# Kernel tuning notes

Hardware: AMD Instinct MI355X
Metric: run time of the kernel (lower is better)

The kernel has to match this reference:

```python
import math
import jax, jax.numpy as jnp
import numpy as np

B, N, C = 2, 2048, 768
H, DH = 12, 64  # num_heads, head_dim


def setup_inputs() -> dict:
    key = jax.random.key(0)
    ks = jax.random.split(key, 5)
    s = 1.0 / math.sqrt(C)  # keep linear outputs O(1)
    return {
        "x": jax.random.normal(ks[0], (B, N, C), jnp.float32),
        "Wq": jax.random.normal(ks[1], (C, C), jnp.float32) * s,
        "bq": jnp.zeros((C,), jnp.float32),
        "Wk": jax.random.normal(ks[2], (C, C), jnp.float32) * s,
        "bk": jnp.zeros((C,), jnp.float32),
        "Wv": jax.random.normal(ks[3], (C, C), jnp.float32) * s,
        "bv": jnp.zeros((C,), jnp.float32),
        "Wp": jax.random.normal(ks[4], (C, C), jnp.float32) * s,
        "bp": jnp.zeros((C,), jnp.float32),
    }


def reference(x, Wq, bq, Wk, bk, Wv, bv, Wp, bp):
    # Linear projections; torch nn.Linear computes x @ W.T + b, here W stored
    # as (in, out) so it's x @ W + b with equivalent math.
    def split(t):  # [B,N,C] -> [B,H,N,DH]
        return t.reshape(B, N, H, DH).transpose(0, 2, 1, 3)

    q = split(x @ Wq + bq)
    k = split(x @ Wk + bk)
    v = split(x @ Wv + bv)
    scale = 1.0 / math.sqrt(DH)
    attn = jnp.einsum("bhqd,bhkd->bhqk", q, k) * scale  # [B,H,N,N]
    attn = jax.nn.softmax(attn, axis=-1)  # attn_drop=0.0 -> identity
    y = jnp.einsum("bhqk,bhkd->bhqd", attn, v)  # [B,H,N,DH]
    y = y.transpose(0, 2, 1, 3).reshape(B, N, C)
    return y @ Wp + bp  # proj_drop=0.0 -> identity
```

## Files before the change

### kernel.cpp

```cpp
#include <hip/hip_runtime.h>


typedef __bf16 bf16_t;
typedef __bf16 bf16x8 __attribute__((ext_vector_type(8)));
typedef __bf16 bf16x4 __attribute__((ext_vector_type(4)));
typedef short  short4_t __attribute__((ext_vector_type(4)));
typedef float  floatx4 __attribute__((ext_vector_type(4)));

#define MFMA32(a, b, c) __builtin_amdgcn_mfma_f32_16x16x32_bf16(a, b, c, 0, 0, 0)
#define MFMA16(a, b, c) __builtin_amdgcn_mfma_f32_16x16x16bf16_1k(a, b, c, 0, 0, 0)

__global__ __launch_bounds__(256) void cvt_x_kernel(const float* __restrict__ x,
                                                    bf16_t* __restrict__ xb) {
  int i = blockIdx.x * 256 + threadIdx.x;
  floatx4 v = ((const floatx4*)x)[i];
  bf16x4 o;
  o[0] = (bf16_t)v[0]; o[1] = (bf16_t)v[1]; o[2] = (bf16_t)v[2]; o[3] = (bf16_t)v[3];
  ((bf16x4*)xb)[i] = o;
}

__global__ __launch_bounds__(256) void cvt_wt_kernel(
    const float* __restrict__ W0, const float* __restrict__ W1,
    const float* __restrict__ W2, const float* __restrict__ W3,
    bf16_t* __restrict__ T0, bf16_t* __restrict__ T1,
    bf16_t* __restrict__ T2, bf16_t* __restrict__ T3) {
  const int z = blockIdx.z;
  const float* W = (z == 0) ? W0 : (z == 1) ? W1 : (z == 2) ? W2 : W3;
  bf16_t* WT = (z == 0) ? T0 : (z == 1) ? T1 : (z == 2) ? T2 : T3;
  __shared__ bf16_t T[64][65];
  const int c = threadIdx.x & 63, r0 = threadIdx.x >> 6;
  const int i0 = blockIdx.y * 64, o0 = blockIdx.x * 64;
#pragma unroll
  for (int p = 0; p < 16; ++p) {
    int r = p * 4 + r0;
    T[r][c] = (bf16_t)W[(i0 + r) * 768 + o0 + c];
  }
  __syncthreads();
#pragma unroll
  for (int p = 0; p < 16; ++p) {
    int r = p * 4 + r0;
    WT[(o0 + r) * 768 + i0 + c] = T[c][r];
  }
}

#define LDPG 72


__global__ __launch_bounds__(256) void gemm_qkv(
    const bf16_t* __restrict__ Xb, const bf16_t* __restrict__ WqT,
    const bf16_t* __restrict__ WkT, const bf16_t* __restrict__ WvT,
    const float* __restrict__ bq, const float* __restrict__ bk,
    const float* __restrict__ bv, bf16_t* __restrict__ qw,
    bf16_t* __restrict__ kw, bf16_t* __restrict__ vtw) {
  __shared__ bf16_t Al[128 * LDPG];
  __shared__ bf16_t Bl[128 * LDPG];
  const int z = blockIdx.z;
  const bf16_t* Wt = (z == 0) ? WqT : (z == 1) ? WkT : WvT;
  const float* bias = (z == 0) ? bq : (z == 1) ? bk : bv;
  const float oscale = (z == 0) ? 0.18033688011112042f : 1.0f;

  const int tid = threadIdx.x, lane = tid & 63, w = tid >> 6;
  const int wr = w >> 1, wc = w & 1;
  const int l15 = lane & 15, quad = lane >> 4;
  const int m0 = blockIdx.y * 128, n0 = blockIdx.x * 128;

  floatx4 acc[4][4] = {};

  for (int kt = 0; kt < 768; kt += 64) {
#pragma unroll
    for (int p = 0; p < 4; ++p) {
      int c = p * 256 + tid;
      int row = c >> 3, qo = (c & 7) * 8;
      *(bf16x8*)&Al[row * LDPG + qo] = *(const bf16x8*)&Wt[(m0 + row) * 768 + kt + qo];
      *(bf16x8*)&Bl[row * LDPG + qo] = *(const bf16x8*)&Xb[(n0 + row) * 768 + kt + qo];
    }
    __syncthreads();
#pragma unroll
    for (int kk = 0; kk < 2; ++kk) {
      bf16x8 af[4], bfr[4];
#pragma unroll
      for (int i = 0; i < 4; ++i) {
        af[i]  = *(bf16x8*)&Al[(wr * 64 + i * 16 + l15) * LDPG + kk * 32 + quad * 8];
        bfr[i] = *(bf16x8*)&Bl[(wc * 64 + i * 16 + l15) * LDPG + kk * 32 + quad * 8];
      }
#pragma unroll
      for (int mi = 0; mi < 4; ++mi)
#pragma unroll
        for (int ni = 0; ni < 4; ++ni)
          acc[mi][ni] = MFMA32(af[mi], bfr[ni], acc[mi][ni]);
    }
    __syncthreads();
  }

  const int hh = (m0 + wr * 64) >> 6;
#pragma unroll
  for (int mi = 0; mi < 4; ++mi) {
    const int d0 = mi * 16 + quad * 4;
    const int gm0 = m0 + wr * 64 + d0;
    float bv4[4];
#pragma unroll
    for (int r = 0; r < 4; ++r) bv4[r] = bias[gm0 + r];
#pragma unroll
    for (int ni = 0; ni < 4; ++ni) {
      const int gn = n0 + wc * 64 + ni * 16 + l15;
      const int bb = gn >> 11, tok = gn & 2047;
      const int bh = bb * 12 + hh;
      if (z == 0) {
        bf16x4 pk;
#pragma unroll
        for (int r = 0; r < 4; ++r)
          pk[r] = (bf16_t)((acc[mi][ni][r] + bv4[r]) * oscale);
        *(bf16x4*)&qw[bh * 131072 + tok * 64 + d0] = pk;
      } else if (z == 1) {
        const int kt2 = tok >> 7, k128 = tok & 127;
        const int nk = k128 >> 4, kl15 = k128 & 15;
        const int kk = d0 >> 5, kq = (d0 >> 3) & 3, j0 = d0 & 7;
        bf16x4 pk;
#pragma unroll
        for (int r = 0; r < 4; ++r)
          pk[r] = (bf16_t)(acc[mi][ni][r] + bv4[r]);
        *(bf16x4*)&kw[bh * 131072 + kt2 * 8192 +
                      ((nk * 2 + kk) * 64 + kq * 16 + kl15) * 8 + j0] = pk;
      } else {
        const int kt2 = tok >> 7, k128 = tok & 127;
        const int nk = k128 >> 4, vq = (k128 >> 2) & 3, j = k128 & 3;
        const int nd = d0 >> 4, vl0 = d0 & 15;
        const int base = bh * 131072 + kt2 * 8192 +
                         ((nk * 4 + nd) * 64 + vq * 16 + vl0) * 4 + j;
#pragma unroll
        for (int r = 0; r < 4; ++r)
          vtw[base + r * 4] = (bf16_t)(acc[mi][ni][r] + bv4[r]);
      }
    }
  }
}

__global__ __launch_bounds__(256) void gemm_proj(
    const bf16_t* __restrict__ Yb, const bf16_t* __restrict__ WpT,
    const float* __restrict__ bias, float* __restrict__ out) {
  __shared__ bf16_t Al[128 * LDPG];
  __shared__ bf16_t Bl[128 * LDPG];
  const int tid = threadIdx.x, lane = tid & 63, w = tid >> 6;
  const int wr = w >> 1, wc = w & 1;
  const int l15 = lane & 15, quad = lane >> 4;
  const int m0 = blockIdx.y * 128, n0 = blockIdx.x * 128;

  floatx4 acc[4][4] = {};

  for (int kt = 0; kt < 768; kt += 64) {
#pragma unroll
    for (int p = 0; p < 4; ++p) {
      int c = p * 256 + tid;
      int row = c >> 3, qo = (c & 7) * 8;
      *(bf16x8*)&Al[row * LDPG + qo] = *(const bf16x8*)&WpT[(m0 + row) * 768 + kt + qo];
      *(bf16x8*)&Bl[row * LDPG + qo] = *(const bf16x8*)&Yb[(n0 + row) * 768 + kt + qo];
    }
    __syncthreads();
#pragma unroll
    for (int kk = 0; kk < 2; ++kk) {
      bf16x8 af[4], bfr[4];
#pragma unroll
      for (int i = 0; i < 4; ++i) {
        af[i]  = *(bf16x8*)&Al[(wr * 64 + i * 16 + l15) * LDPG + kk * 32 + quad * 8];
        bfr[i] = *(bf16x8*)&Bl[(wc * 64 + i * 16 + l15) * LDPG + kk * 32 + quad * 8];
      }
#pragma unroll
      for (int mi = 0; mi < 4; ++mi)
#pragma unroll
        for (int ni = 0; ni < 4; ++ni)
          acc[mi][ni] = MFMA32(af[mi], bfr[ni], acc[mi][ni]);
    }
    __syncthreads();
  }

#pragma unroll
  for (int mi = 0; mi < 4; ++mi) {
    const int gm0 = m0 + wr * 64 + mi * 16 + quad * 4;
    floatx4 bv4;
#pragma unroll
    for (int r = 0; r < 4; ++r) bv4[r] = bias[gm0 + r];
#pragma unroll
    for (int ni = 0; ni < 4; ++ni) {
      const int gn = n0 + wc * 64 + ni * 16 + l15;
      floatx4 v = acc[mi][ni] + bv4;
      *(floatx4*)&out[gn * 768 + gm0] = v;
    }
  }
}

__global__ __launch_bounds__(256, 4) void attn_kernel(
    const bf16_t* __restrict__ Q, const bf16_t* __restrict__ Kf,
    const bf16_t* __restrict__ Vf, bf16_t* __restrict__ Y) {
  __shared__ __align__(16) bf16_t smem[16384];
  __shared__ float Ls[2][2][2][16];
  bf16_t* Kl = smem;
  bf16_t* Vl = smem + 8192;
  float* Ox = (float*)smem;

  const int tid = threadIdx.x, lane = tid & 63, w = tid >> 6;
  const int wq = w & 1, wk = w >> 1;
  const int l15 = lane & 15, quad = lane >> 4;
  const int bh = blockIdx.y;
  const int q0 = blockIdx.x * 64;
  const bf16_t* Qb = Q + bh * 131072;
  const bf16_t* Kb = Kf + bh * 131072;
  const bf16_t* Vb = Vf + bh * 131072;

  bf16x8 qf[2][2];
#pragma unroll
  for (int ni = 0; ni < 2; ++ni)
#pragma unroll
    for (int kk = 0; kk < 2; ++kk)
      qf[ni][kk] = *(const bf16x8*)&Qb[(q0 + wq * 32 + ni * 16 + l15) * 64 +
                                       kk * 32 + quad * 8];

  floatx4 oacc[2][4] = {};
  float lsum[2] = {0.f, 0.f};

  for (int kt = 0; kt < 16; ++kt) {
    const bf16_t* kg = Kb + kt * 8192;
    const bf16_t* vg = Vb + kt * 8192;
#pragma unroll
    for (int p = 0; p < 4; ++p) {
      const int off = (p * 256 + tid) * 8;
      *(bf16x8*)&Kl[off] = *(const bf16x8*)&kg[off];
      *(bf16x8*)&Vl[off] = *(const bf16x8*)&vg[off];
    }
    __syncthreads();

    short4_t pk[4][2];
#pragma unroll
    for (int mt = 0; mt < 4; ++mt) {
      floatx4 s[2] = {};
#pragma unroll
      for (int kk = 0; kk < 2; ++kk) {
        bf16x8 kfr = *(bf16x8*)&Kl[((wk * 4 + mt) * 2 + kk) * 512 + lane * 8];
#pragma unroll
        for (int ni = 0; ni < 2; ++ni)
          s[ni] = MFMA32(kfr, qf[ni][kk], s[ni]);
      }
#pragma unroll
      for (int ni = 0; ni < 2; ++ni) {
        bf16x4 ph;
#pragma unroll
        for (int r = 0; r < 4; ++r) {
          const float pv = __builtin_amdgcn_exp2f(s[ni][r]);
          lsum[ni] += pv;
          ph[r] = (bf16_t)pv;
        }
        pk[mt][ni] = __builtin_bit_cast(short4_t, ph);
      }
    }

#pragma unroll
    for (int mt = 0; mt < 4; ++mt)
#pragma unroll
      for (int nd = 0; nd < 4; ++nd) {
        bf16x4 vfr = *(bf16x4*)&Vl[((wk * 4 + mt) * 4 + nd) * 256 + lane * 4];
        short4_t vs = __builtin_bit_cast(short4_t, vfr);
#pragma unroll
        for (int ni = 0; ni < 2; ++ni)
          oacc[ni][nd] = MFMA16(pk[mt][ni], vs, oacc[ni][nd]);
      }
    __syncthreads();
  }

#pragma unroll
  for (int ni = 0; ni < 2; ++ni) {
    lsum[ni] += __shfl_xor(lsum[ni], 16);
    lsum[ni] += __shfl_xor(lsum[ni], 32);
  }
  if (quad == 0) {
#pragma unroll
    for (int ni = 0; ni < 2; ++ni) Ls[wq][wk][ni][l15] = lsum[ni];
  }

#pragma unroll
  for (int ni = 0; ni < 2; ++ni)
#pragma unroll
    for (int ndl = 0; ndl < 2; ++ndl) {
      const int nd = (1 - wk) * 2 + ndl;
      *(floatx4*)&Ox[((((wq * 2 + wk) * 2 + ni) * 2 + ndl) * 64 + lane) * 4] =
          oacc[ni][nd];
    }
  __syncthreads();

  const int bb = bh / 12, h = bh % 12;
#pragma unroll
  for (int ni = 0; ni < 2; ++ni) {
    float tot[4];
#pragma unroll
    for (int r = 0; r < 4; ++r)
      tot[r] = Ls[wq][0][ni][quad * 4 + r] + Ls[wq][1][ni][quad * 4 + r];
#pragma unroll
    for (int ndl = 0; ndl < 2; ++ndl) {
      const int nd = wk * 2 + ndl;
      floatx4 o = oacc[ni][nd];
      floatx4 other =
          *(floatx4*)&Ox[((((wq * 2 + (1 - wk)) * 2 + ni) * 2 + ndl) * 64 + lane) * 4];
      o += other;
#pragma unroll
      for (int r = 0; r < 4; ++r) {
        const int tok = q0 + wq * 32 + ni * 16 + quad * 4 + r;
        const int col = h * 64 + nd * 16 + l15;
        Y[(bb * 2048 + tok) * 768 + col] = (bf16_t)(o[r] / tot[r]);
      }
    }
  }
}

extern "C" void kernel_launch(void* const* d_in, const int* in_sizes, int n_in,
                              void* d_out, int out_size, void* d_ws, size_t ws_size,
                              hipStream_t stream) {
  const float* x  = (const float*)d_in[0];
  const float* Wq = (const float*)d_in[1];
  const float* bq = (const float*)d_in[2];
  const float* Wk = (const float*)d_in[3];
  const float* bk = (const float*)d_in[4];
  const float* Wv = (const float*)d_in[5];
  const float* bv = (const float*)d_in[6];
  const float* Wp = (const float*)d_in[7];
  const float* bp = (const float*)d_in[8];
  float* out = (float*)d_out;

  char* ws = (char*)d_ws;
  bf16_t* xb  = (bf16_t*)ws; ws += (size_t)4096 * 768 * 2;
  bf16_t* WqT = (bf16_t*)ws; ws += (size_t)768 * 768 * 2;
  bf16_t* WkT = (bf16_t*)ws; ws += (size_t)768 * 768 * 2;
  bf16_t* WvT = (bf16_t*)ws; ws += (size_t)768 * 768 * 2;
  bf16_t* WpT = (bf16_t*)ws; ws += (size_t)768 * 768 * 2;
  bf16_t* qw  = (bf16_t*)ws; ws += (size_t)24 * 2048 * 64 * 2;
  bf16_t* kw  = (bf16_t*)ws; ws += (size_t)24 * 2048 * 64 * 2;
  bf16_t* vtw = (bf16_t*)ws; ws += (size_t)24 * 2048 * 64 * 2;
  bf16_t* yw  = (bf16_t*)ws; ws += (size_t)4096 * 768 * 2;

  cvt_x_kernel<<<3072, 256, 0, stream>>>(x, xb);
  cvt_wt_kernel<<<dim3(12, 12, 4), 256, 0, stream>>>(Wq, Wk, Wv, Wp, WqT, WkT, WvT, WpT);

  gemm_qkv<<<dim3(32, 6, 3), 256, 0, stream>>>(xb, WqT, WkT, WvT, bq, bk, bv, qw, kw, vtw);
  attn_kernel<<<dim3(32, 24), 256, 0, stream>>>(qw, kw, vtw, yw);
  gemm_proj<<<dim3(32, 6), 256, 0, stream>>>(yw, WpT, bp, out);
}
```

Before: 189.4 us.

## Load attention K/V fragments directly from global and use direct-to-LDS GEMM loads

The attention kernel drops the shared-memory staging of K and V tiles. Each wave loads its pre-laid-out fragments from global memory into registers, which removes two block barriers per tile, and MFMA sections are bracketed with s_setprio. The QKV and projection GEMMs now fill LDS with global_load_lds 16-byte direct loads and drop the padded row stride. The trade-offs are more register pressure (occupancy hint lowered to 3), redundant K/V global reads across blocks that depend on cache hits, and possible LDS bank conflicts from the unpadded 64-element stride.

New measurement: 193.9 us. +2.4%, slower.

```diff
diff --git a/kernel.cpp b/kernel.cpp
--- a/kernel.cpp
+++ b/kernel.cpp
@@ -9,6 +9,12 @@
 
 #define MFMA32(a, b, c) __builtin_amdgcn_mfma_f32_16x16x32_bf16(a, b, c, 0, 0, 0)
 #define MFMA16(a, b, c) __builtin_amdgcn_mfma_f32_16x16x16bf16_1k(a, b, c, 0, 0, 0)
+
+__device__ __forceinline__ void gload16(const bf16_t* g, bf16_t* l) {
+  __builtin_amdgcn_global_load_lds(
+      (__attribute__((address_space(1))) void*)g,
+      (__attribute__((address_space(3))) void*)l, 16, 0, 0);
+}
 
 __global__ __launch_bounds__(256) void cvt_x_kernel(const float* __restrict__ x,
                                                     bf16_t* __restrict__ xb) {
@@ -43,8 +49,6 @@
   }
 }
 
-#define LDPG 72
-
 
 __global__ __launch_bounds__(256) void gemm_qkv(
     const bf16_t* __restrict__ Xb, const bf16_t* __restrict__ WqT,
@@ -52,8 +56,8 @@
     const float* __restrict__ bq, const float* __restrict__ bk,
     const float* __restrict__ bv, bf16_t* __restrict__ qw,
     bf16_t* __restrict__ kw, bf16_t* __restrict__ vtw) {
-  __shared__ bf16_t Al[128 * LDPG];
-  __shared__ bf16_t Bl[128 * LDPG];
+  __shared__ bf16_t Al[128 * 64];
+  __shared__ bf16_t Bl[128 * 64];
   const int z = blockIdx.z;
   const bf16_t* Wt = (z == 0) ? WqT : (z == 1) ? WkT : WvT;
   const float* bias = (z == 0) ? bq : (z == 1) ? bk : bv;
@@ -64,15 +68,18 @@
   const int l15 = lane & 15, quad = lane >> 4;
   const int m0 = blockIdx.y * 128, n0 = blockIdx.x * 128;
 
+  const bf16_t* ga = &Wt[(m0 + w * 32 + (lane >> 3)) * 768 + (lane & 7) * 8];
+  const bf16_t* gb = &Xb[(n0 + w * 32 + (lane >> 3)) * 768 + (lane & 7) * 8];
+  bf16_t* la = &Al[w * 32 * 64];
+  bf16_t* lb = &Bl[w * 32 * 64];
+
   floatx4 acc[4][4] = {};
 
   for (int kt = 0; kt < 768; kt += 64) {
 #pragma unroll
     for (int p = 0; p < 4; ++p) {
-      int c = p * 256 + tid;
-      int row = c >> 3, qo = (c & 7) * 8;
-      *(bf16x8*)&Al[row * LDPG + qo] = *(const bf16x8*)&Wt[(m0 + row) * 768 + kt + qo];
-      *(bf16x8*)&Bl[row * LDPG + qo] = *(const bf16x8*)&Xb[(n0 + row) * 768 + kt + qo];
+      gload16(ga + p * 8 * 768 + kt, la + p * 8 * 64);
+      gload16(gb + p * 8 * 768 + kt, lb + p * 8 * 64);
     }
     __syncthreads();
 #pragma unroll
@@ -80,8 +87,8 @@
       bf16x8 af[4], bfr[4];
 #pragma unroll
       for (int i = 0; i < 4; ++i) {
-        af[i]  = *(bf16x8*)&Al[(wr * 64 + i * 16 + l15) * LDPG + kk * 32 + quad * 8];
-        bfr[i] = *(bf16x8*)&Bl[(wc * 64 + i * 16 + l15) * LDPG + kk * 32 + quad * 8];
+        af[i]  = *(bf16x8*)&Al[(wr * 64 + i * 16 + l15) * 64 + kk * 32 + quad * 8];
+        bfr[i] = *(bf16x8*)&Bl[(wc * 64 + i * 16 + l15) * 64 + kk * 32 + quad * 8];
       }
 #pragma unroll
       for (int mi = 0; mi < 4; ++mi)
@@ -138,22 +145,25 @@
 __global__ __launch_bounds__(256) void gemm_proj(
     const bf16_t* __restrict__ Yb, const bf16_t* __restrict__ WpT,
     const float* __restrict__ bias, float* __restrict__ out) {
-  __shared__ bf16_t Al[128 * LDPG];
-  __shared__ bf16_t Bl[128 * LDPG];
+  __shared__ bf16_t Al[128 * 64];
+  __shared__ bf16_t Bl[128 * 64];
   const int tid = threadIdx.x, lane = tid & 63, w = tid >> 6;
   const int wr = w >> 1, wc = w & 1;
   const int l15 = lane & 15, quad = lane >> 4;
   const int m0 = blockIdx.y * 128, n0 = blockIdx.x * 128;
 
+  const bf16_t* ga = &WpT[(m0 + w * 32 + (lane >> 3)) * 768 + (lane & 7) * 8];
+  const bf16_t* gb = &Yb[(n0 + w * 32 + (lane >> 3)) * 768 + (lane & 7) * 8];
+  bf16_t* la = &Al[w * 32 * 64];
+  bf16_t* lb = &Bl[w * 32 * 64];
+
   floatx4 acc[4][4] = {};
 
   for (int kt = 0; kt < 768; kt += 64) {
 #pragma unroll
     for (int p = 0; p < 4; ++p) {
-      int c = p * 256 + tid;
-      int row = c >> 3, qo = (c & 7) * 8;
-      *(bf16x8*)&Al[row * LDPG + qo] = *(const bf16x8*)&WpT[(m0 + row) * 768 + kt + qo];
-      *(bf16x8*)&Bl[row * LDPG + qo] = *(const bf16x8*)&Yb[(n0 + row) * 768 + kt + qo];
+      gload16(ga + p * 8 * 768 + kt, la + p * 8 * 64);
+      gload16(gb + p * 8 * 768 + kt, lb + p * 8 * 64);
     }
     __syncthreads();
 #pragma unroll
@@ -161,8 +171,8 @@
       bf16x8 af[4], bfr[4];
 #pragma unroll
       for (int i = 0; i < 4; ++i) {
-        af[i]  = *(bf16x8*)&Al[(wr * 64 + i * 16 + l15) * LDPG + kk * 32 + quad * 8];
-        bfr[i] = *(bf16x8*)&Bl[(wc * 64 + i * 16 + l15) * LDPG + kk * 32 + quad * 8];
+        af[i]  = *(bf16x8*)&Al[(wr * 64 + i * 16 + l15) * 64 + kk * 32 + quad * 8];
+        bfr[i] = *(bf16x8*)&Bl[(wc * 64 + i * 16 + l15) * 64 + kk * 32 + quad * 8];
       }
 #pragma unroll
       for (int mi = 0; mi < 4; ++mi)
@@ -188,14 +198,11 @@
   }
 }
 
-__global__ __launch_bounds__(256, 4) void attn_kernel(
+__global__ __launch_bounds__(256, 3) void attn_kernel(
     const bf16_t* __restrict__ Q, const bf16_t* __restrict__ Kf,
     const bf16_t* __restrict__ Vf, bf16_t* __restrict__ Y) {
-  __shared__ __align__(16) bf16_t smem[16384];
+  __shared__ __align__(16) float Ox[4096];
   __shared__ float Ls[2][2][2][16];
-  bf16_t* Kl = smem;
-  bf16_t* Vl = smem + 8192;
-  float* Ox = (float*)smem;
 
   const int tid = threadIdx.x, lane = tid & 63, w = tid >> 6;
   const int wq = w & 1, wk = w >> 1;
@@ -203,8 +210,8 @@
   const int bh = blockIdx.y;
   const int q0 = blockIdx.x * 64;
   const bf16_t* Qb = Q + bh * 131072;
-  const bf16_t* Kb = Kf + bh * 131072;
-  const bf16_t* Vb = Vf + bh * 131072;
+  const bf16_t* Kb = Kf + bh * 131072 + wk * 4096 + lane * 8;
+  const bf16_t* Vb = Vf + bh * 131072 + wk * 4096 + lane * 4;
 
   bf16x8 qf[2][2];
 #pragma unroll
@@ -220,25 +227,31 @@
   for (int kt = 0; kt < 16; ++kt) {
     const bf16_t* kg = Kb + kt * 8192;
     const bf16_t* vg = Vb + kt * 8192;
-#pragma unroll
-    for (int p = 0; p < 4; ++p) {
-      const int off = (p * 256 + tid) * 8;
-      *(bf16x8*)&Kl[off] = *(const bf16x8*)&kg[off];
-      *(bf16x8*)&Vl[off] = *(const bf16x8*)&vg[off];
-    }
-    __syncthreads();
+
+    bf16x8 kfr[4][2];
+#pragma unroll
+    for (int mt = 0; mt < 4; ++mt)
+#pragma unroll
+      for (int kk = 0; kk < 2; ++kk)
+        kfr[mt][kk] = *(const bf16x8*)&kg[(mt * 2 + kk) * 512];
+    bf16x4 vfr[4][4];
+#pragma unroll
+    for (int mt = 0; mt < 4; ++mt)
+#pragma unroll
+      for (int nd = 0; nd < 4; ++nd)
+        vfr[mt][nd] = *(const bf16x4*)&vg[(mt * 4 + nd) * 256];
 
     short4_t pk[4][2];
 #pragma unroll
     for (int mt = 0; mt < 4; ++mt) {
       floatx4 s[2] = {};
-#pragma unroll
-      for (int kk = 0; kk < 2; ++kk) {
-        bf16x8 kfr = *(bf16x8*)&Kl[((wk * 4 + mt) * 2 + kk) * 512 + lane * 8];
+      __builtin_amdgcn_s_setprio(1);
+#pragma unroll
+      for (int kk = 0; kk < 2; ++kk)
 #pragma unroll
         for (int ni = 0; ni < 2; ++ni)
-          s[ni] = MFMA32(kfr, qf[ni][kk], s[ni]);
-      }
+          s[ni] = MFMA32(kfr[mt][kk], qf[ni][kk], s[ni]);
+      __builtin_amdgcn_s_setprio(0);
 #pragma unroll
       for (int ni = 0; ni < 2; ++ni) {
         bf16x4 ph;
@@ -252,17 +265,17 @@
       }
     }
 
+    __builtin_amdgcn_s_setprio(1);
 #pragma unroll
     for (int mt = 0; mt < 4; ++mt)
 #pragma unroll
       for (int nd = 0; nd < 4; ++nd) {
-        bf16x4 vfr = *(bf16x4*)&Vl[((wk * 4 + mt) * 4 + nd) * 256 + lane * 4];
-        short4_t vs = __builtin_bit_cast(short4_t, vfr);
+        short4_t vs = __builtin_bit_cast(short4_t, vfr[mt][nd]);
 #pragma unroll
         for (int ni = 0; ni < 2; ++ni)
           oacc[ni][nd] = MFMA16(pk[mt][ni], vs, oacc[ni][nd]);
       }
-    __syncthreads();
+    __builtin_amdgcn_s_setprio(0);
   }
 
 #pragma unroll
```
